# Kernel tuning notes

Hardware: AMD Instinct MI355X
Metric: run time of the kernel (lower is better)

Reference implementation:

```python
import jax, jax.numpy as jnp
import numpy as np

DIM = 256
NUM_HEADS = 8
HEAD_DIM = DIM // NUM_HEADS
WS = 7                 # window_size
N = WS * WS            # tokens per window
B = 4096               # batch * num_windows


def _make_rel_index(ws):
    coords = np.stack(np.meshgrid(np.arange(ws), np.arange(ws), indexing='ij'))  # [2,ws,ws]
    cf = coords.reshape(2, -1)                                                   # [2,N]
    rel = cf[:, :, None] - cf[:, None, :]                                        # [2,N,N]
    rel = rel.transpose(1, 2, 0).copy()
    rel[:, :, 0] += ws - 1
    rel[:, :, 1] += ws - 1
    rel[:, :, 0] *= 2 * ws - 1
    return rel.sum(-1).astype(np.int32)                                          # [N,N]


def setup_inputs() -> dict:
    key = jax.random.key(0)
    ks = jax.random.split(key, 6)
    x = jax.random.normal(ks[0], (B, N, DIM), dtype=jnp.float32)
    qkv_w = jax.random.normal(ks[1], (3 * DIM, DIM), dtype=jnp.float32) * 0.02
    qkv_b = jax.random.normal(ks[2], (3 * DIM,), dtype=jnp.float32) * 0.02
    proj_w = jax.random.normal(ks[3], (DIM, DIM), dtype=jnp.float32) * 0.02
    proj_b = jax.random.normal(ks[4], (DIM,), dtype=jnp.float32) * 0.02
    bias_table = jax.random.normal(ks[5], ((2 * WS - 1) ** 2, NUM_HEADS), dtype=jnp.float32) * 0.02
    rel_index = jnp.asarray(_make_rel_index(WS))
    return {"x": x, "qkv_w": qkv_w, "qkv_b": qkv_b, "proj_w": proj_w,
            "proj_b": proj_b, "bias_table": bias_table, "rel_index": rel_index}


def reference(x, qkv_w, qkv_b, proj_w, proj_b, bias_table, rel_index):
    B_, n, C = x.shape
    scale = HEAD_DIM ** (-0.5)
    # qkv projection -> [3, B, H, N, hd]
    qkv = (x @ qkv_w.T + qkv_b).reshape(B_, n, 3, NUM_HEADS, HEAD_DIM)
    qkv = qkv.transpose(2, 0, 3, 1, 4)
    q, k, v = qkv[0], qkv[1], qkv[2]
    attn = jnp.einsum('bhnd,bhmd->bhnm', q * scale, k)
    # relative position bias gather: [N,N,H] -> [1,H,N,N]
    rel_bias = bias_table[rel_index]                       # [N,N,H]
    attn = attn + rel_bias.transpose(2, 0, 1)[None]
    attn = jax.nn.softmax(attn, axis=-1)
    out = jnp.einsum('bhnm,bhmd->bhnd', attn, v)           # [B,H,N,hd]
    out = out.transpose(0, 2, 1, 3).reshape(B_, n, C)
    return out @ proj_w.T + proj_b
```

## Files before the change

kernel.cpp:

```cpp
#include <hip/hip_runtime.h>
#include <hip/hip_bf16.h>
#include <stdint.h>

#define NWIN 4096

typedef __attribute__((ext_vector_type(8))) short bf16x8;
typedef __attribute__((ext_vector_type(4))) float f32x4;

#define OFF_WQ 0LL
#define OFF_WP 393216LL
#define OFF_RB 524288LL
#define OFF_B  655360LL
#define OFF_Q  1048576LL
#define QKV_STRIDE 102760448LL
#define OFF_K  (OFF_Q + QKV_STRIDE)
#define OFF_V  (OFF_Q + 2 * QKV_STRIDE)

static __device__ __forceinline__ uint32_t f2bf(float f) {
    union { float f; uint32_t u; } v; v.f = f;
    return (v.u + 0x7FFFu + ((v.u >> 16) & 1u)) >> 16;
}

static __device__ __forceinline__ uint32_t pk2(float lo, float hi) {
    union { __hip_bfloat162 h; uint32_t u; } c;
    c.h = __float22bfloat162_rn(float2{lo, hi});
    return c.u;
}

union FragU { uint32_t u[4]; bf16x8 v; };

__global__ void prep_kernel(const float* __restrict__ qkv_w, const float* __restrict__ proj_w,
                            const float* __restrict__ qkv_b,
                            const float* __restrict__ bias_table, const int* __restrict__ rel_index,
                            char* __restrict__ ws) {
    uint16_t* wq  = (uint16_t*)(ws + OFF_WQ);
    uint16_t* wp  = (uint16_t*)(ws + OFF_WP);
    float*    rb  = (float*)(ws + OFF_RB);
    float*    wsb = (float*)(ws + OFF_B);
    const int total = 196608 + 65536 + 32768 + 768;
    for (int idx = blockIdx.x * blockDim.x + threadIdx.x; idx < total;
         idx += gridDim.x * blockDim.x) {
        if (idx < 196608) {
            wq[idx] = (uint16_t)f2bf(qkv_w[idx]);
        } else if (idx < 262144) {
            int i = idx - 196608;
            wp[i] = (uint16_t)f2bf(proj_w[i]);
        } else if (idx < 294912) {
            int i = idx - 262144;
            int h = i >> 12, kt4 = (i >> 8) & 15, qt = (i >> 2) & 63, ii = i & 3;
            int kt = kt4 * 4 + ii;
            float v = -1e30f;
            if (kt < 49 && qt < 49)
                v = bias_table[rel_index[qt * 49 + kt] * 8 + h] * 1.4426950408889634f;
            rb[i] = v;
        } else {
            int n = idx - 294912;
            wsb[n] = qkv_b[n];
        }
    }
}

__global__ __launch_bounds__(256, 2) void qkv_kernel(const float* __restrict__ x,
                                                     char* __restrict__ ws) {
    __shared__ __align__(16) char smem[32768];
    uint16_t* A  = (uint16_t*)smem;
    uint16_t* Bt = (uint16_t*)(smem + 16384);
    const uint16_t* wq  = (const uint16_t*)(ws + OFF_WQ);
    const float*    wsb = (const float*)(ws + OFF_B);
    const int P = blockIdx.x;
    const int s = P / 48, r = P % 48;
    const int g = s * 8 + (r & 7);
    const int m0 = g * 128, n0 = (r >> 3) * 128;
    const int t = threadIdx.x, l = t & 63, w = t >> 6;
    const int lr = l & 15, lg = l >> 4;
    const int wm = w >> 1, wn = w & 1;
    f32x4 acc[4][4];
    #pragma unroll
    for (int a = 0; a < 4; ++a)
        #pragma unroll
        for (int b2 = 0; b2 < 4; ++b2) acc[a][b2] = (f32x4){0.f, 0.f, 0.f, 0.f};

    for (int kk = 0; kk < 4; ++kk) {
        #pragma unroll
        for (int it = 0; it < 4; ++it) {
            int item = it * 256 + t;
            int rr = item >> 3, ch = item & 7;
            const float* src = x + (int64_t)(m0 + rr) * 256 + kk * 64 + ch * 8;
            float4 v0 = *(const float4*)src;
            float4 v1 = *(const float4*)(src + 4);
            uint4 pk;
            pk.x = pk2(v0.x, v0.y); pk.y = pk2(v0.z, v0.w);
            pk.z = pk2(v1.x, v1.y); pk.w = pk2(v1.z, v1.w);
            *(uint4*)((char*)A + ((rr * 128 + ch * 16) ^ ((rr & 7) << 4))) = pk;
        }
        #pragma unroll
        for (int it = 0; it < 4; ++it) {
            int item = it * 256 + t;
            int rr = item >> 3, ch = item & 7;
            uint4 v = *(const uint4*)(wq + (int64_t)(n0 + rr) * 256 + kk * 64 + ch * 8);
            *(uint4*)((char*)Bt + ((rr * 128 + ch * 16) ^ ((rr & 7) << 4))) = v;
        }
        __syncthreads();
        #pragma unroll
        for (int kh = 0; kh < 2; ++kh) {
            bf16x8 af[4], bfr[4];
            #pragma unroll
            for (int mi = 0; mi < 4; ++mi) {
                int rr = wm * 64 + 16 * mi + lr;
                af[mi] = *(const bf16x8*)((char*)A + ((rr * 128 + kh * 64 + lg * 16) ^ ((rr & 7) << 4)));
            }
            #pragma unroll
            for (int nj = 0; nj < 4; ++nj) {
                int rr = wn * 64 + 16 * nj + lr;
                bfr[nj] = *(const bf16x8*)((char*)Bt + ((rr * 128 + kh * 64 + lg * 16) ^ ((rr & 7) << 4)));
            }
            #pragma unroll
            for (int nj = 0; nj < 4; ++nj)
                #pragma unroll
                for (int mi = 0; mi < 4; ++mi)
                    acc[nj][mi] = __builtin_amdgcn_mfma_f32_16x16x32_bf16(bfr[nj], af[mi], acc[nj][mi], 0, 0, 0);
        }
        __syncthreads();
    }
    uint16_t* C = (uint16_t*)smem;
    #pragma unroll
    for (int nj = 0; nj < 4; ++nj) {
        f32x4 bias = *(const f32x4*)(wsb + n0 + wn * 64 + 16 * nj + 4 * lg);
        #pragma unroll
        for (int mi = 0; mi < 4; ++mi) {
            int tok_l = wm * 64 + 16 * mi + lr;
            int nb = wn * 64 + 16 * nj + 4 * lg;
            uint2 pk;
            pk.x = pk2(acc[nj][mi][0] + bias[0], acc[nj][mi][1] + bias[1]);
            pk.y = pk2(acc[nj][mi][2] + bias[2], acc[nj][mi][3] + bias[3]);
            *(uint2*)((char*)C + ((tok_l * 256 + nb * 2) ^ ((tok_l & 7) << 4))) = pk;
        }
    }
    __syncthreads();
    const int sel = n0 >> 8;
    char* dstBase = ws + OFF_Q + (int64_t)sel * QKV_STRIDE;
    #pragma unroll
    for (int it = 0; it < 8; ++it) {
        int hh = it >> 1;
        int mrow = ((it & 1) << 6) | (t >> 2);
        int q4 = t & 3;
        uint4 v = *(const uint4*)((char*)C + ((mrow * 256 + hh * 64 + q4 * 16) ^ ((mrow & 7) << 4)));
        int m = m0 + mrow;
        int b = m / 49;
        int tok = m - b * 49;
        int h = ((n0 >> 5) + hh) & 7;
        *(uint4*)(dstBase + (((int64_t)b * 8 + h) * 49 + tok) * 64 + q4 * 16) = v;
    }
}

__global__ __launch_bounds__(512, 2) void attn_kernel(const float* __restrict__ proj_b,
                                                      float* __restrict__ out,
                                                      const char* __restrict__ ws) {
    __shared__ __align__(16) char smem[32768];
    const int b = blockIdx.x;
    const int t = threadIdx.x, l = t & 63, w = t >> 6;
    const int lr = l & 15, lg = l >> 4;
    const uint16_t* Q = (const uint16_t*)(ws + OFF_Q);
    const uint16_t* K = (const uint16_t*)(ws + OFF_K);
    const uint16_t* V = (const uint16_t*)(ws + OFF_V);
    const uint16_t* wp = (const uint16_t*)(ws + OFF_WP);
    const float*   rb = (const float*)(ws + OFF_RB);
    char* VL = smem + w * 4096;
    char* OL = smem;
    const float scale = 0.17677669529663687f * 1.4426950408889634f;
    const int64_t bh = (int64_t)b * 8 + w;

    uint4 vstage[4];
    int   vc[4];
    #pragma unroll
    for (int it = 0; it < 4; ++it) {
        int item = it * 64 + l;
        int tok = item >> 2, d0 = (item & 3) * 8;
        int a = tok >> 4, g = (tok >> 2) & 3, ii = tok & 3;
        vc[it] = (a >> 1) * 32 + g * 8 + (a & 1) * 4 + ii;
        uint4 v = {0u, 0u, 0u, 0u};
        if (tok < 49) v = *(const uint4*)(V + (bh * 49 + tok) * 32 + d0);
        vstage[it] = v;
    }

    bf16x8 qf[4], kf[4];
    #pragma unroll
    for (int nj = 0; nj < 4; ++nj)
        qf[nj] = *(const bf16x8*)(Q + (bh * 49 + 16 * nj + lr) * 32 + lg * 8);
    #pragma unroll
    for (int mj = 0; mj < 4; ++mj)
        kf[mj] = *(const bf16x8*)(K + (bh * 49 + 16 * mj + lr) * 32 + lg * 8);

    float rs[4];
    bf16x8 pf[4][2];
    #pragma unroll
    for (int nj = 0; nj < 4; ++nj) {
        f32x4 s[4];
        __builtin_amdgcn_s_setprio(1);
        #pragma unroll
        for (int mj = 0; mj < 4; ++mj)
            s[mj] = __builtin_amdgcn_mfma_f32_16x16x32_bf16(
                kf[mj], qf[nj], (f32x4){0.f, 0.f, 0.f, 0.f}, 0, 0, 0);
        __builtin_amdgcn_s_setprio(0);
        #pragma unroll
        for (int mj = 0; mj < 4; ++mj) {
            f32x4 rbv = *(const f32x4*)(rb + ((w * 16 + 4 * mj + lg) * 64 + 16 * nj + lr) * 4);
            s[mj] = s[mj] * scale + rbv;
        }
        float m = s[0][0];
        #pragma unroll
        for (int mj = 0; mj < 4; ++mj)
            #pragma unroll
            for (int i = 0; i < 4; ++i) m = fmaxf(m, s[mj][i]);
        m = fmaxf(m, __shfl_xor(m, 16));
        m = fmaxf(m, __shfl_xor(m, 32));
        float sum = 0.f;
        #pragma unroll
        for (int mj = 0; mj < 4; ++mj)
            #pragma unroll
            for (int i = 0; i < 4; ++i) {
                float e = __builtin_amdgcn_exp2f(s[mj][i] - m);
                s[mj][i] = e;
                sum += e;
            }
        sum += __shfl_xor(sum, 16);
        sum += __shfl_xor(sum, 32);
        rs[nj] = sum;
        #pragma unroll
        for (int ks = 0; ks < 2; ++ks) {
            FragU f;
            f.u[0] = pk2(s[2 * ks][0], s[2 * ks][1]);
            f.u[1] = pk2(s[2 * ks][2], s[2 * ks][3]);
            f.u[2] = pk2(s[2 * ks + 1][0], s[2 * ks + 1][1]);
            f.u[3] = pk2(s[2 * ks + 1][2], s[2 * ks + 1][3]);
            pf[nj][ks] = f.v;
        }
    }

    #pragma unroll
    for (int it = 0; it < 4; ++it) {
        int item = it * 64 + l;
        int d0 = (item & 3) * 8;
        int c = vc[it];
        const uint32_t words[4] = {vstage[it].x, vstage[it].y, vstage[it].z, vstage[it].w};
        #pragma unroll
        for (int jj = 0; jj < 4; ++jj) {
            int dA = d0 + 2 * jj, dB = dA + 1;
            *(uint16_t*)(VL + ((dA * 128 + c * 2) ^ ((dA & 7) << 4))) = (uint16_t)words[jj];
            *(uint16_t*)(VL + ((dB * 128 + c * 2) ^ ((dB & 7) << 4))) = (uint16_t)(words[jj] >> 16);
        }
    }
    bf16x8 vf[2][2];
    #pragma unroll
    for (int dt = 0; dt < 2; ++dt)
        #pragma unroll
        for (int ks = 0; ks < 2; ++ks) {
            int row = dt * 16 + lr;
            vf[dt][ks] = *(const bf16x8*)(VL + ((row * 128 + ks * 64 + lg * 16) ^ ((row & 7) << 4)));
        }

    f32x4 o[2][4];
    __builtin_amdgcn_s_setprio(1);
    #pragma unroll
    for (int dt = 0; dt < 2; ++dt)
        #pragma unroll
        for (int nj = 0; nj < 4; ++nj) {
            f32x4 acc = __builtin_amdgcn_mfma_f32_16x16x32_bf16(
                vf[dt][0], pf[nj][0], (f32x4){0.f, 0.f, 0.f, 0.f}, 0, 0, 0);
            o[dt][nj] = __builtin_amdgcn_mfma_f32_16x16x32_bf16(vf[dt][1], pf[nj][1], acc, 0, 0, 0);
        }
    __builtin_amdgcn_s_setprio(0);

    __syncthreads();
    #pragma unroll
    for (int nj = 0; nj < 4; ++nj) {
        const float rinv = 1.0f / rs[nj];
        const int row = 16 * nj + lr;
        const int swz = (row & 7) << 4;
        #pragma unroll
        for (int dt = 0; dt < 2; ++dt) {
            uint2 pk;
            pk.x = pk2(o[dt][nj][0] * rinv, o[dt][nj][1] * rinv);
            pk.y = pk2(o[dt][nj][2] * rinv, o[dt][nj][3] * rinv);
            *(uint2*)(OL + ((row * 512 + w * 64 + dt * 32 + lg * 8) ^ swz)) = pk;
        }
    }
    __syncthreads();

    f32x4 pacc[4][2];
    #pragma unroll
    for (int mi = 0; mi < 4; ++mi)
        #pragma unroll
        for (int nj = 0; nj < 2; ++nj)
            pacc[mi][nj] = (f32x4){0.f, 0.f, 0.f, 0.f};
    #pragma unroll
    for (int kk = 0; kk < 8; ++kk) {
        bf16x8 av[4];
        #pragma unroll
        for (int mi = 0; mi < 4; ++mi) {
            const int row = mi * 16 + lr;
            av[mi] = *(const bf16x8*)(OL + ((row * 512 + kk * 64 + lg * 16) ^ ((row & 7) << 4)));
        }
        #pragma unroll
        for (int nj = 0; nj < 2; ++nj) {
            bf16x8 bv = *(const bf16x8*)(wp + (w * 32 + nj * 16 + lr) * 256 + kk * 32 + lg * 8);
            #pragma unroll
            for (int mi = 0; mi < 4; ++mi)
                pacc[mi][nj] = __builtin_amdgcn_mfma_f32_16x16x32_bf16(av[mi], bv, pacc[mi][nj], 0, 0, 0);
        }
    }
    #pragma unroll
    for (int nj = 0; nj < 2; ++nj) {
        const int n = w * 32 + nj * 16 + lr;
        const float pb = proj_b[n];
        #pragma unroll
        for (int mi = 0; mi < 4; ++mi)
            #pragma unroll
            for (int i = 0; i < 4; ++i) {
                const int tok = mi * 16 + lg * 4 + i;
                if (tok < 49)
                    out[((int64_t)b * 49 + tok) * 256 + n] = pacc[mi][nj][i] + pb;
            }
    }
}

extern "C" void kernel_launch(void* const* d_in, const int* in_sizes, int n_in,
                              void* d_out, int out_size, void* d_ws, size_t ws_size,
                              hipStream_t stream) {
    const float* x          = (const float*)d_in[0];
    const float* qkv_w      = (const float*)d_in[1];
    const float* qkv_b      = (const float*)d_in[2];
    const float* proj_w     = (const float*)d_in[3];
    const float* proj_b     = (const float*)d_in[4];
    const float* bias_table = (const float*)d_in[5];
    const int*   rel_index  = (const int*)d_in[6];
    float* out = (float*)d_out;
    char*  ws  = (char*)d_ws;

    prep_kernel<<<1155, 256, 0, stream>>>(qkv_w, proj_w, qkv_b, bias_table, rel_index, ws);
    qkv_kernel<<<9408, 256, 0, stream>>>(x, ws);
    attn_kernel<<<NWIN, 512, 0, stream>>>(proj_b, out, ws);
}
```

Measured before the change: 315.5 us.

## Double-buffer QKV GEMM shared tiles with register prefetch of next K slice

The QKV projection GEMM now loads the next K-slice of x and weights into registers while MFMAs run on the current shared-memory buffer, then writes it to a second LDS buffer. This is meant to hide global load latency behind compute and cut one barrier per iteration. In exchange, LDS use doubles to 64KB per block and register pressure rises, which may reduce occupancy below the two blocks per CU requested by the launch bounds.

```diff
diff --git a/kernel.cpp b/kernel.cpp
--- a/kernel.cpp
+++ b/kernel.cpp
@@ -62,9 +62,7 @@
 
 __global__ __launch_bounds__(256, 2) void qkv_kernel(const float* __restrict__ x,
                                                      char* __restrict__ ws) {
-    __shared__ __align__(16) char smem[32768];
-    uint16_t* A  = (uint16_t*)smem;
-    uint16_t* Bt = (uint16_t*)(smem + 16384);
+    __shared__ __align__(16) char smem[65536];
     const uint16_t* wq  = (const uint16_t*)(ws + OFF_WQ);
     const float*    wsb = (const float*)(ws + OFF_B);
     const int P = blockIdx.x;
@@ -74,45 +72,62 @@
     const int t = threadIdx.x, l = t & 63, w = t >> 6;
     const int lr = l & 15, lg = l >> 4;
     const int wm = w >> 1, wn = w & 1;
+    const int srow = t >> 3, sch = t & 7;
+
     f32x4 acc[4][4];
     #pragma unroll
     for (int a = 0; a < 4; ++a)
         #pragma unroll
         for (int b2 = 0; b2 < 4; ++b2) acc[a][b2] = (f32x4){0.f, 0.f, 0.f, 0.f};
 
+    float4 va[4][2];
+    uint4  vb4[4];
+
+    #pragma unroll
+    for (int it = 0; it < 4; ++it) {
+        int rrow = it * 32 + srow;
+        const float* src = x + (int64_t)(m0 + rrow) * 256 + sch * 8;
+        va[it][0] = *(const float4*)src;
+        va[it][1] = *(const float4*)(src + 4);
+        vb4[it]   = *(const uint4*)(wq + (int64_t)(n0 + rrow) * 256 + sch * 8);
+    }
+    #pragma unroll
+    for (int it = 0; it < 4; ++it) {
+        int rrow = it * 32 + srow;
+        uint4 pk;
+        pk.x = pk2(va[it][0].x, va[it][0].y); pk.y = pk2(va[it][0].z, va[it][0].w);
+        pk.z = pk2(va[it][1].x, va[it][1].y); pk.w = pk2(va[it][1].z, va[it][1].w);
+        int off = (rrow * 128 + sch * 16) ^ ((rrow & 7) << 4);
+        *(uint4*)(smem + off) = pk;
+        *(uint4*)(smem + 16384 + off) = vb4[it];
+    }
+    __syncthreads();
+
+    #pragma unroll
     for (int kk = 0; kk < 4; ++kk) {
-        #pragma unroll
-        for (int it = 0; it < 4; ++it) {
-            int item = it * 256 + t;
-            int rr = item >> 3, ch = item & 7;
-            const float* src = x + (int64_t)(m0 + rr) * 256 + kk * 64 + ch * 8;
-            float4 v0 = *(const float4*)src;
-            float4 v1 = *(const float4*)(src + 4);
-            uint4 pk;
-            pk.x = pk2(v0.x, v0.y); pk.y = pk2(v0.z, v0.w);
-            pk.z = pk2(v1.x, v1.y); pk.w = pk2(v1.z, v1.w);
-            *(uint4*)((char*)A + ((rr * 128 + ch * 16) ^ ((rr & 7) << 4))) = pk;
-        }
-        #pragma unroll
-        for (int it = 0; it < 4; ++it) {
-            int item = it * 256 + t;
-            int rr = item >> 3, ch = item & 7;
-            uint4 v = *(const uint4*)(wq + (int64_t)(n0 + rr) * 256 + kk * 64 + ch * 8);
-            *(uint4*)((char*)Bt + ((rr * 128 + ch * 16) ^ ((rr & 7) << 4))) = v;
-        }
-        __syncthreads();
+        char* cur = smem + (kk & 1) * 32768;
+        if (kk < 3) {
+            #pragma unroll
+            for (int it = 0; it < 4; ++it) {
+                int rrow = it * 32 + srow;
+                const float* src = x + (int64_t)(m0 + rrow) * 256 + (kk + 1) * 64 + sch * 8;
+                va[it][0] = *(const float4*)src;
+                va[it][1] = *(const float4*)(src + 4);
+                vb4[it]   = *(const uint4*)(wq + (int64_t)(n0 + rrow) * 256 + (kk + 1) * 64 + sch * 8);
+            }
+        }
         #pragma unroll
         for (int kh = 0; kh < 2; ++kh) {
             bf16x8 af[4], bfr[4];
             #pragma unroll
             for (int mi = 0; mi < 4; ++mi) {
-                int rr = wm * 64 + 16 * mi + lr;
-                af[mi] = *(const bf16x8*)((char*)A + ((rr * 128 + kh * 64 + lg * 16) ^ ((rr & 7) << 4)));
+                int rr2 = wm * 64 + 16 * mi + lr;
+                af[mi] = *(const bf16x8*)(cur + ((rr2 * 128 + kh * 64 + lg * 16) ^ ((rr2 & 7) << 4)));
             }
             #pragma unroll
             for (int nj = 0; nj < 4; ++nj) {
-                int rr = wn * 64 + 16 * nj + lr;
-                bfr[nj] = *(const bf16x8*)((char*)Bt + ((rr * 128 + kh * 64 + lg * 16) ^ ((rr & 7) << 4)));
+                int rr2 = wn * 64 + 16 * nj + lr;
+                bfr[nj] = *(const bf16x8*)(cur + 16384 + ((rr2 * 128 + kh * 64 + lg * 16) ^ ((rr2 & 7) << 4)));
             }
             #pragma unroll
             for (int nj = 0; nj < 4; ++nj)
@@ -120,8 +135,22 @@
                 for (int mi = 0; mi < 4; ++mi)
                     acc[nj][mi] = __builtin_amdgcn_mfma_f32_16x16x32_bf16(bfr[nj], af[mi], acc[nj][mi], 0, 0, 0);
         }
+        if (kk < 3) {
+            char* nxt = smem + ((kk + 1) & 1) * 32768;
+            #pragma unroll
+            for (int it = 0; it < 4; ++it) {
+                int rrow = it * 32 + srow;
+                uint4 pk;
+                pk.x = pk2(va[it][0].x, va[it][0].y); pk.y = pk2(va[it][0].z, va[it][0].w);
+                pk.z = pk2(va[it][1].x, va[it][1].y); pk.w = pk2(va[it][1].z, va[it][1].w);
+                int off = (rrow * 128 + sch * 16) ^ ((rrow & 7) << 4);
+                *(uint4*)(nxt + off) = pk;
+                *(uint4*)(nxt + 16384 + off) = vb4[it];
+            }
+        }
         __syncthreads();
     }
+
     uint16_t* C = (uint16_t*)smem;
     #pragma unroll
     for (int nj = 0; nj < 4; ++nj) {
```

Measured after the change: 388.2 us. +23.0%, slower.

## Pre-swizzle QKV weights and load weight tiles directly to LDS

Applied to the files above, without the earlier changes.

The prep kernel now writes the bf16 QKV weights in a tiled, pre-swizzled layout that matches the LDS layout of the GEMM B tile. The QKV kernel then uses global_load_lds to copy each 16 KB weight tile straight into shared memory, skipping the register round trip and per-thread address swizzling. This is meant to cut VGPR traffic and instruction count in the load phase. It relies on direct-to-LDS loads completing before the barrier, which is a correctness risk if the wait counts are not handled.

```diff
diff --git a/kernel.cpp b/kernel.cpp
--- a/kernel.cpp
+++ b/kernel.cpp
@@ -33,7 +33,7 @@
                             const float* __restrict__ qkv_b,
                             const float* __restrict__ bias_table, const int* __restrict__ rel_index,
                             char* __restrict__ ws) {
-    uint16_t* wq  = (uint16_t*)(ws + OFF_WQ);
+    uint16_t* wqs = (uint16_t*)(ws + OFF_WQ);
     uint16_t* wp  = (uint16_t*)(ws + OFF_WP);
     float*    rb  = (float*)(ws + OFF_RB);
     float*    wsb = (float*)(ws + OFF_B);
@@ -41,7 +41,14 @@
     for (int idx = blockIdx.x * blockDim.x + threadIdx.x; idx < total;
          idx += gridDim.x * blockDim.x) {
         if (idx < 196608) {
-            wq[idx] = (uint16_t)f2bf(qkv_w[idx]);
+            int p  = idx;
+            int e  = p & 7;
+            int ch = (p >> 3) & 7;
+            int rr = (p >> 6) & 127;
+            int kk = (p >> 13) & 3;
+            int jt = p >> 15;
+            int src = (jt * 128 + rr) * 256 + kk * 64 + ((ch ^ (rr & 7)) * 8) + e;
+            wqs[p] = (uint16_t)f2bf(qkv_w[src]);
         } else if (idx < 262144) {
             int i = idx - 196608;
             wp[i] = (uint16_t)f2bf(proj_w[i]);
@@ -63,10 +70,10 @@
 __global__ __launch_bounds__(256, 2) void qkv_kernel(const float* __restrict__ x,
                                                      char* __restrict__ ws) {
     __shared__ __align__(16) char smem[32768];
-    uint16_t* A  = (uint16_t*)smem;
-    uint16_t* Bt = (uint16_t*)(smem + 16384);
-    const uint16_t* wq  = (const uint16_t*)(ws + OFF_WQ);
-    const float*    wsb = (const float*)(ws + OFF_B);
+    uint16_t* A = (uint16_t*)smem;
+    char*     Bt = smem + 16384;
+    const char*  wqs = ws + OFF_WQ;
+    const float* wsb = (const float*)(ws + OFF_B);
     const int P = blockIdx.x;
     const int s = P / 48, r = P % 48;
     const int g = s * 8 + (r & 7);
@@ -80,7 +87,18 @@
         #pragma unroll
         for (int b2 = 0; b2 < 4; ++b2) acc[a][b2] = (f32x4){0.f, 0.f, 0.f, 0.f};
 
+    const int jt = n0 >> 7;
+
     for (int kk = 0; kk < 4; ++kk) {
+        {
+            const char* bsrc = wqs + (((int64_t)(jt * 4 + kk)) << 14) + w * 1024 + l * 16;
+            #pragma unroll
+            for (int it = 0; it < 4; ++it)
+                __builtin_amdgcn_global_load_lds(
+                    (const __attribute__((address_space(1))) void*)(bsrc + it * 4096),
+                    (__attribute__((address_space(3))) void*)(Bt + it * 4096 + w * 1024),
+                    16, 0, 0);
+        }
         #pragma unroll
         for (int it = 0; it < 4; ++it) {
             int item = it * 256 + t;
@@ -93,26 +111,19 @@
             pk.z = pk2(v1.x, v1.y); pk.w = pk2(v1.z, v1.w);
             *(uint4*)((char*)A + ((rr * 128 + ch * 16) ^ ((rr & 7) << 4))) = pk;
         }
-        #pragma unroll
-        for (int it = 0; it < 4; ++it) {
-            int item = it * 256 + t;
-            int rr = item >> 3, ch = item & 7;
-            uint4 v = *(const uint4*)(wq + (int64_t)(n0 + rr) * 256 + kk * 64 + ch * 8);
-            *(uint4*)((char*)Bt + ((rr * 128 + ch * 16) ^ ((rr & 7) << 4))) = v;
-        }
         __syncthreads();
         #pragma unroll
         for (int kh = 0; kh < 2; ++kh) {
             bf16x8 af[4], bfr[4];
             #pragma unroll
             for (int mi = 0; mi < 4; ++mi) {
-                int rr = wm * 64 + 16 * mi + lr;
-                af[mi] = *(const bf16x8*)((char*)A + ((rr * 128 + kh * 64 + lg * 16) ^ ((rr & 7) << 4)));
+                int rr2 = wm * 64 + 16 * mi + lr;
+                af[mi] = *(const bf16x8*)((char*)A + ((rr2 * 128 + kh * 64 + lg * 16) ^ ((rr2 & 7) << 4)));
             }
             #pragma unroll
             for (int nj = 0; nj < 4; ++nj) {
-                int rr = wn * 64 + 16 * nj + lr;
-                bfr[nj] = *(const bf16x8*)((char*)Bt + ((rr * 128 + kh * 64 + lg * 16) ^ ((rr & 7) << 4)));
+                int rr2 = wn * 64 + 16 * nj + lr;
+                bfr[nj] = *(const bf16x8*)(Bt + ((rr2 * 128 + kh * 64 + lg * 16) ^ ((rr2 & 7) << 4)));
             }
             #pragma unroll
             for (int nj = 0; nj < 4; ++nj)
```

New measurement: 353.5 us. 12.0% more time.
